# Performance work log

Measured on AMD Instinct MI355X. Metric: run time of the kernel, lower is better.

The kernel has to match this reference:

```python
import jax, jax.numpy as jnp
import numpy as np

R, K, H_IN, W_IN = 512, 17, 56, 56   # rois, keypoints, heatmap size
ROI_H = ROI_W = 96                   # = ceil(BOX_LEN), fixed by construction
BOX_LEN = 95.5                       # all boxes have this side length
A = -0.75                            # PyTorch bicubic coefficient


def _cubic(x):
    x = jnp.abs(x)
    near = ((A + 2.0) * x - (A + 3.0)) * x * x + 1.0
    far = A * (((x - 5.0) * x + 8.0) * x - 4.0)
    return jnp.where(x <= 1.0, near, jnp.where(x < 2.0, far, 0.0))


def _resize_matrix(out_size, in_size):
    """Dense [out,in] bicubic interpolation matrix (align_corners=False, border-replicate)."""
    scale = in_size / out_size
    src = (jnp.arange(out_size, dtype=jnp.float32) + 0.5) * scale - 0.5
    base = jnp.floor(src).astype(jnp.int32)
    taps = base[:, None] + jnp.arange(-1, 3)                      # [out, 4]
    w = _cubic(src[:, None] - taps.astype(jnp.float32))           # weights from unclamped dist
    taps = jnp.clip(taps, 0, in_size - 1)                         # replicate border
    rows = jnp.broadcast_to(jnp.arange(out_size)[:, None], taps.shape)
    return jnp.zeros((out_size, in_size), jnp.float32).at[rows, taps].add(w)


def setup_inputs() -> dict:
    key = jax.random.key(0)
    k1, k2 = jax.random.split(key)
    masks = jax.random.normal(k1, (R, K, H_IN, W_IN), dtype=jnp.float32)
    offs = jax.random.uniform(k2, (R, 2), jnp.float32, 0.0, 400.0)
    # corner format (c0_start, c1_start, c0_end, c1_end); all lengths == BOX_LEN
    boxes = jnp.concatenate([offs, offs + BOX_LEN], axis=1)
    return {"masks": masks, "boxes": boxes}


def reference(masks, boxes):
    My = _resize_matrix(ROI_H, H_IN)   # [ROI_H, H_IN]
    Mx = _resize_matrix(ROI_W, W_IN)   # [ROI_W, W_IN]
    # separable bicubic resize of every ROI heatmap: [R,K,ROI_H,ROI_W]
    roi = jnp.einsum('hi,rkij,wj->rkhw', My, masks, Mx)
    flat = roi.reshape(R, K, ROI_H * ROI_W)
    pos = jnp.argmax(flat, axis=-1)                                # [R,K]
    y = pos // ROI_W
    x = pos % ROI_W
    scores = jnp.take_along_axis(flat, pos[..., None], axis=-1)[..., 0]  # logit at argmax
    len0 = jnp.maximum(boxes[:, 2] - boxes[:, 0], 1.0)
    len1 = jnp.maximum(boxes[:, 3] - boxes[:, 1], 1.0)
    corr0 = (len0 / ROI_H)[:, None]
    corr1 = (len1 / ROI_W)[:, None]
    p0 = (y.astype(jnp.float32) + 0.5) * corr0 + boxes[:, 0:1]
    p1 = (x.astype(jnp.float32) + 0.5) * corr1 + boxes[:, 1:2]
    predictions = jnp.stack([p0, p1, jnp.ones_like(p0)], axis=1)   # [R, n_dim+1, K]
    return predictions, scores
```

## Files before the change

### kernel.cpp

```cpp
#include <hip/hip_runtime.h>

#define R_    512
#define K_    17
#define HIN   56
#define WIN   56
#define OUTS  96
#define NMAP  (R_ * K_)
#define NT    192
#define RST   98
#define TROWS 60

typedef float v2f __attribute__((ext_vector_type(2)));

constexpr float cubic_c(float xin) {
    float x = xin < 0.0f ? -xin : xin;
    const float A = -0.75f;
    if (x <= 1.0f) return ((A + 2.0f) * x - (A + 3.0f)) * x * x + 1.0f;
    if (x < 2.0f)  return A * (((x - 5.0f) * x + 8.0f) * x - 4.0f);
    return 0.0f;
}

struct XTabT {
    float w[OUTS][4];
    int   s[OUTS];
    constexpr XTabT() : w{}, s{} {
        for (int o = 0; o < OUTS; ++o) {
            float src = ((float)o + 0.5f) * (56.0f / 96.0f) - 0.5f;
            int base = (int)src;
            if ((float)base > src) --base;
            int st = base - 1;
            if (st < 0) st = 0;
            if (st > HIN - 4) st = HIN - 4;
            s[o] = st;
            for (int q = 0; q < 4; ++q) {
                int tap = base - 1 + q;
                float wt = cubic_c(src - (float)tap);
                int p = tap < 0 ? 0 : (tap > HIN - 1 ? HIN - 1 : tap);
                w[o][p - st] += wt;
            }
        }
    }
};
constexpr XTabT XT;

struct YTabT {
    float w[12][4];
    int   d[12];
    constexpr YTabT() : w{}, d{} {
        for (int ph = 0; ph < 12; ++ph) {
            float src = ((float)ph + 0.5f) * (56.0f / 96.0f) - 0.5f;
            int base = (int)src;
            if ((float)base > src) --base;
            d[ph] = base - 1;
            for (int q = 0; q < 4; ++q)
                w[ph][q] = cubic_c(src - (float)(base - 1 + q));
        }
    }
};
constexpr YTabT YT;

template<int G>
__device__ __forceinline__ void p1_cols(const float* __restrict__ r0,
                                        const float* __restrict__ r1,
                                        v2f* __restrict__ dst) {
    constexpr int FS = (G == 0) ? 0 : (G == 1) ? 4 : 9;
    constexpr int NF = (G == 1) ? 6 : 5;
    v2f rr[NF * 4];
    const float4* A = (const float4*)r0 + FS;
    const float4* B = (const float4*)r1 + FS;
#pragma unroll
    for (int i = 0; i < NF; ++i) {
        float4 a = A[i], b = B[i];
        rr[4 * i + 0] = (v2f){a.x, b.x};
        rr[4 * i + 1] = (v2f){a.y, b.y};
        rr[4 * i + 2] = (v2f){a.z, b.z};
        rr[4 * i + 3] = (v2f){a.w, b.w};
    }
#pragma unroll
    for (int i = 0; i < 16; ++i) {
        const int o0 = 32 * G + 2 * i, o1 = o0 + 1;
        const int s0 = XT.s[o0] - 4 * FS, s1 = XT.s[o1] - 4 * FS;
        v2f a0 = rr[s0] * (v2f){XT.w[o0][0], XT.w[o0][0]};
        a0 = __builtin_elementwise_fma((v2f){XT.w[o0][1], XT.w[o0][1]}, rr[s0 + 1], a0);
        a0 = __builtin_elementwise_fma((v2f){XT.w[o0][2], XT.w[o0][2]}, rr[s0 + 2], a0);
        a0 = __builtin_elementwise_fma((v2f){XT.w[o0][3], XT.w[o0][3]}, rr[s0 + 3], a0);
        v2f a1 = rr[s1] * (v2f){XT.w[o1][0], XT.w[o1][0]};
        a1 = __builtin_elementwise_fma((v2f){XT.w[o1][1], XT.w[o1][1]}, rr[s1 + 1], a1);
        a1 = __builtin_elementwise_fma((v2f){XT.w[o1][2], XT.w[o1][2]}, rr[s1 + 2], a1);
        a1 = __builtin_elementwise_fma((v2f){XT.w[o1][3], XT.w[o1][3]}, rr[s1 + 3], a1);
        float4 st = {a0.x, a0.y, a1.x, a1.y};
        *(float4*)(dst + 2 * i) = st;
    }
}

__device__ __forceinline__ v2f yv(const v2f* __restrict__ c, int hh) {
    const int ph = hh % 12, b = hh / 12;
    const int i0 = 7 * b + YT.d[ph] + 2;
    v2f acc = c[i0] * (v2f){YT.w[ph][0], YT.w[ph][0]};
    acc = __builtin_elementwise_fma((v2f){YT.w[ph][1], YT.w[ph][1]}, c[i0 + 1], acc);
    acc = __builtin_elementwise_fma((v2f){YT.w[ph][2], YT.w[ph][2]}, c[i0 + 2], acc);
    acc = __builtin_elementwise_fma((v2f){YT.w[ph][3], YT.w[ph][3]}, c[i0 + 3], acc);
    return acc;
}

__global__ __launch_bounds__(NT)
void _Keypointer_kernel(const float* __restrict__ masks,
                        const float* __restrict__ boxes,
                        float* __restrict__ out) {
    __shared__ __align__(16) v2f tmp[TROWS * RST];
    __shared__ v2f wmax[3];
    __shared__ int candp[2];

    const int t   = threadIdx.x;
    const int bm0 = 2 * blockIdx.x;
    const int g   = t >> 6;
    const int w   = t & 63;

    const int srcrow = min(max(w - 2, 0), HIN - 1);
    const int phys   = min(w, TROWS - 1);
    const float* r0 = masks + (size_t)bm0 * (HIN * WIN) + srcrow * WIN;
    const float* r1 = r0 + HIN * WIN;
    v2f* dst = tmp + phys * RST + 32 * g;
    if      (g == 0) p1_cols<0>(r0, r1, dst);
    else if (g == 1) p1_cols<1>(r0, r1, dst);
    else             p1_cols<2>(r0, r1, dst);

    if (t == 0) { candp[0] = 0x7fffffff; candp[1] = 0x7fffffff; }
    __syncthreads();

    const int half = (t >= 96) ? 1 : 0;
    const int col  = t - 96 * half;
    const int h0   = 48 * half;
    const v2f* cb  = tmp + (28 * half) * RST + col;
    v2f c[32];
#pragma unroll
    for (int i = 0; i < 32; ++i) c[i] = cb[i * RST];

    v2f vmax = {-INFINITY, -INFINITY};
#pragma unroll
    for (int hh = 0; hh < 48; ++hh)
        vmax = __builtin_elementwise_max(vmax, yv(c, hh));

    float m0 = vmax.x, m1 = vmax.y;
#pragma unroll
    for (int off = 32; off > 0; off >>= 1) {
        m0 = fmaxf(m0, __shfl_down(m0, off, 64));
        m1 = fmaxf(m1, __shfl_down(m1, off, 64));
    }
    if (w == 0) wmax[g] = (v2f){m0, m1};
    __syncthreads();

    const float M0 = fmaxf(fmaxf(wmax[0].x, wmax[1].x), wmax[2].x);
    const float M1 = fmaxf(fmaxf(wmax[0].y, wmax[1].y), wmax[2].y);

    if (vmax.x == M0 || vmax.y == M1) {
        int c0 = 0x7fffffff, c1 = 0x7fffffff;
#pragma unroll
        for (int hh = 0; hh < 48; ++hh) {
            v2f a = yv(c, hh);
            int fp = (h0 + hh) * OUTS + col;
            if (a.x == M0) c0 = min(c0, fp);
            if (a.y == M1) c1 = min(c1, fp);
        }
        if (c0 != 0x7fffffff) atomicMin(&candp[0], c0);
        if (c1 != 0x7fffffff) atomicMin(&candp[1], c1);
    }
    __syncthreads();

    if (t < 2) {
        const int map = bm0 + t;
        const float M = t ? M1 : M0;
        const int bp  = candp[t];
        const int r = map / K_, k = map - r * K_;
        const int y = bp / OUTS, x = bp - y * OUTS;
        const float b0f = boxes[r * 4 + 0], b1f = boxes[r * 4 + 1];
        const float b2f = boxes[r * 4 + 2], b3f = boxes[r * 4 + 3];
        const float corr0 = fmaxf(b2f - b0f, 1.0f) / (float)OUTS;
        const float corr1 = fmaxf(b3f - b1f, 1.0f) / (float)OUTS;
        const float p0 = ((float)y + 0.5f) * corr0 + b0f;
        const float p1 = ((float)x + 0.5f) * corr1 + b1f;
        out[(r * 3 + 0) * K_ + k] = p0;
        out[(r * 3 + 1) * K_ + k] = p1;
        out[(r * 3 + 2) * K_ + k] = 1.0f;
        out[R_ * 3 * K_ + r * K_ + k] = M;
    }
}

extern "C" void kernel_launch(void* const* d_in, const int* in_sizes, int n_in,
                              void* d_out, int out_size, void* d_ws, size_t ws_size,
                              hipStream_t stream) {
    const float* masks = (const float*)d_in[0];
    const float* boxes = (const float*)d_in[1];
    float* out = (float*)d_out;
    _Keypointer_kernel<<<NMAP / 2, NT, 0, stream>>>(masks, boxes, out);
}
```

Measured before the change: 158.3 us.

## Stage masks through LDS with coalesced loads and process rows in two halves

The kernel now loads both input maps into shared memory with coalesced float4 reads instead of having each thread fetch whole rows straight from global memory. The horizontal pass is split into two 32-row halves that reuse a smaller tmp buffer, and the vertical pass runs in matching halves. Launch bounds ask for 3 blocks per CU. This trades extra syncs and a larger LDS footprint (about 26KB staging plus 25KB tmp) for better global coalescing and fewer registers per thread.

```diff
diff --git a/kernel.cpp b/kernel.cpp
--- a/kernel.cpp
+++ b/kernel.cpp
@@ -8,7 +8,8 @@
 #define NMAP  (R_ * K_)
 #define NT    192
 #define RST   98
-#define TROWS 60
+#define SROW  58
+#define SMAP  (HIN * SROW)
 
 typedef float v2f __attribute__((ext_vector_type(2)));
 
@@ -60,21 +61,23 @@
 constexpr YTabT YT;
 
 template<int G>
-__device__ __forceinline__ void p1_cols(const float* __restrict__ r0,
-                                        const float* __restrict__ r1,
+__device__ __forceinline__ void p1_cols(const float* __restrict__ sa,
+                                        const float* __restrict__ sb,
                                         v2f* __restrict__ dst) {
     constexpr int FS = (G == 0) ? 0 : (G == 1) ? 4 : 9;
     constexpr int NF = (G == 1) ? 6 : 5;
     v2f rr[NF * 4];
-    const float4* A = (const float4*)r0 + FS;
-    const float4* B = (const float4*)r1 + FS;
-#pragma unroll
-    for (int i = 0; i < NF; ++i) {
-        float4 a = A[i], b = B[i];
-        rr[4 * i + 0] = (v2f){a.x, b.x};
-        rr[4 * i + 1] = (v2f){a.y, b.y};
-        rr[4 * i + 2] = (v2f){a.z, b.z};
-        rr[4 * i + 3] = (v2f){a.w, b.w};
+    {
+        float a_[NF * 4], b_[NF * 4];
+#pragma unroll
+        for (int p = 0; p < NF * 2; ++p) {
+            float2 va = *(const float2*)(sa + 2 * p);
+            float2 vb = *(const float2*)(sb + 2 * p);
+            a_[2 * p] = va.x; a_[2 * p + 1] = va.y;
+            b_[2 * p] = vb.x; b_[2 * p + 1] = vb.y;
+        }
+#pragma unroll
+        for (int f = 0; f < NF * 4; ++f) rr[f] = (v2f){a_[f], b_[f]};
     }
 #pragma unroll
     for (int i = 0; i < 16; ++i) {
@@ -88,9 +91,22 @@
         a1 = __builtin_elementwise_fma((v2f){XT.w[o1][1], XT.w[o1][1]}, rr[s1 + 1], a1);
         a1 = __builtin_elementwise_fma((v2f){XT.w[o1][2], XT.w[o1][2]}, rr[s1 + 2], a1);
         a1 = __builtin_elementwise_fma((v2f){XT.w[o1][3], XT.w[o1][3]}, rr[s1 + 3], a1);
-        float4 st = {a0.x, a0.y, a1.x, a1.y};
-        *(float4*)(dst + 2 * i) = st;
-    }
+        *(float4*)(dst + 2 * i) = (float4){a0.x, a0.y, a1.x, a1.y};
+    }
+}
+
+__device__ __forceinline__ void p1_half(const float* __restrict__ stg,
+                                        v2f* __restrict__ tmp, int t, bool low) {
+    const int g = t >> 6;
+    const int w = t & 63;
+    if (w >= 32) return;
+    const int srcrow = low ? max(w - 2, 0) : min(26 + w, HIN - 1);
+    const float* sa = stg + srcrow * SROW + ((g == 0) ? 0 : (g == 1) ? 16 : 36);
+    const float* sb = sa + SMAP;
+    v2f* dst = tmp + w * RST + 32 * g;
+    if      (g == 0) p1_cols<0>(sa, sb, dst);
+    else if (g == 1) p1_cols<1>(sa, sb, dst);
+    else             p1_cols<2>(sa, sb, dst);
 }
 
 __device__ __forceinline__ v2f yv(const v2f* __restrict__ c, int hh) {
@@ -103,43 +119,62 @@
     return acc;
 }
 
-__global__ __launch_bounds__(NT)
+__global__ __launch_bounds__(NT, 3)
 void _Keypointer_kernel(const float* __restrict__ masks,
                         const float* __restrict__ boxes,
                         float* __restrict__ out) {
-    __shared__ __align__(16) v2f tmp[TROWS * RST];
+    __shared__ __align__(16) float stg[2 * SMAP];
+    __shared__ __align__(16) v2f  tmp[32 * RST];
     __shared__ v2f wmax[3];
     __shared__ int candp[2];
 
     const int t   = threadIdx.x;
     const int bm0 = 2 * blockIdx.x;
-    const int g   = t >> 6;
-    const int w   = t & 63;
-
-    const int srcrow = min(max(w - 2, 0), HIN - 1);
-    const int phys   = min(w, TROWS - 1);
-    const float* r0 = masks + (size_t)bm0 * (HIN * WIN) + srcrow * WIN;
-    const float* r1 = r0 + HIN * WIN;
-    v2f* dst = tmp + phys * RST + 32 * g;
-    if      (g == 0) p1_cols<0>(r0, r1, dst);
-    else if (g == 1) p1_cols<1>(r0, r1, dst);
-    else             p1_cols<2>(r0, r1, dst);
-
+
+    {
+        const float4* g4 = (const float4*)(masks + (size_t)bm0 * (HIN * WIN));
+        int u = t, mm = 0, r = t / 14, kk = t % 14;
+#pragma unroll
+        for (int i = 0; i < 9; ++i) {
+            if (i < 8 || u < 1568) {
+                float4 v = g4[u];
+                float* d = stg + mm * SMAP + r * SROW + 4 * kk;
+                *(float2*)(d)     = make_float2(v.x, v.y);
+                *(float2*)(d + 2) = make_float2(v.z, v.w);
+            }
+            u += NT;
+            kk += 10; if (kk >= 14) { kk -= 14; ++r; }
+            r += 13;  if (r >= HIN) { r -= HIN; mm = 1; }
+        }
+    }
     if (t == 0) { candp[0] = 0x7fffffff; candp[1] = 0x7fffffff; }
     __syncthreads();
 
-    const int half = (t >= 96) ? 1 : 0;
-    const int col  = t - 96 * half;
-    const int h0   = 48 * half;
-    const v2f* cb  = tmp + (28 * half) * RST + col;
-    v2f c[32];
-#pragma unroll
-    for (int i = 0; i < 32; ++i) c[i] = cb[i * RST];
+    const int qq  = t / 96;
+    const int col = t - 96 * qq;
+    const v2f* cb = tmp + 14 * qq * RST + col;
+
+    p1_half(stg, tmp, t, true);
+    __syncthreads();
+    v2f c_lo[18];
+#pragma unroll
+    for (int i = 0; i < 18; ++i) c_lo[i] = cb[i * RST];
+    __syncthreads();
+
+    p1_half(stg, tmp, t, false);
 
     v2f vmax = {-INFINITY, -INFINITY};
 #pragma unroll
-    for (int hh = 0; hh < 48; ++hh)
-        vmax = __builtin_elementwise_max(vmax, yv(c, hh));
+    for (int hh = 0; hh < 24; ++hh)
+        vmax = __builtin_elementwise_max(vmax, yv(c_lo, hh));
+    __syncthreads();
+
+    v2f c_hi[18];
+#pragma unroll
+    for (int i = 0; i < 18; ++i) c_hi[i] = cb[i * RST];
+#pragma unroll
+    for (int hh = 0; hh < 24; ++hh)
+        vmax = __builtin_elementwise_max(vmax, yv(c_hi, hh));
 
     float m0 = vmax.x, m1 = vmax.y;
 #pragma unroll
@@ -147,7 +182,7 @@
         m0 = fmaxf(m0, __shfl_down(m0, off, 64));
         m1 = fmaxf(m1, __shfl_down(m1, off, 64));
     }
-    if (w == 0) wmax[g] = (v2f){m0, m1};
+    if ((t & 63) == 0) wmax[t >> 6] = (v2f){m0, m1};
     __syncthreads();
 
     const float M0 = fmaxf(fmaxf(wmax[0].x, wmax[1].x), wmax[2].x);
@@ -156,9 +191,16 @@
     if (vmax.x == M0 || vmax.y == M1) {
         int c0 = 0x7fffffff, c1 = 0x7fffffff;
 #pragma unroll
-        for (int hh = 0; hh < 48; ++hh) {
-            v2f a = yv(c, hh);
-            int fp = (h0 + hh) * OUTS + col;
+        for (int hh = 0; hh < 24; ++hh) {
+            v2f a = yv(c_lo, hh);
+            int fp = (24 * qq + hh) * OUTS + col;
+            if (a.x == M0) c0 = min(c0, fp);
+            if (a.y == M1) c1 = min(c1, fp);
+        }
+#pragma unroll
+        for (int hh = 0; hh < 24; ++hh) {
+            v2f a = yv(c_hi, hh);
+            int fp = (48 + 24 * qq + hh) * OUTS + col;
             if (a.x == M0) c0 = min(c0, fp);
             if (a.y == M1) c1 = min(c1, fp);
         }
```

Result: slower. 169.0 us (+6.7%).

## Process four map pairs per block with register prefetch of next pair

Applied to the files above, without the earlier changes.

Each block now loops over four map pairs, loading the next pair's mask rows into registers while computing the current pair's horizontal pass and argmax. Barriers are replaced by a lighter LDS-only waitcnt+barrier, and launch bounds request two blocks per CU. This aims to hide global load latency and amortise block launch overhead, at the cost of a quarter as many blocks and more register pressure.

```diff
diff --git a/kernel.cpp b/kernel.cpp
--- a/kernel.cpp
+++ b/kernel.cpp
@@ -8,9 +8,18 @@
 #define NMAP  (R_ * K_)
 #define NT    192
 #define RST   98
-#define TROWS 60
+#define MAPSZ (HIN * WIN)
+#define PAIRS 4
+#define NBLK  (NMAP / (2 * PAIRS))
 
 typedef float v2f __attribute__((ext_vector_type(2)));
+
+__device__ __forceinline__ void bar_lds() {
+    asm volatile("" ::: "memory");
+    __builtin_amdgcn_s_waitcnt(0xc07f);
+    __builtin_amdgcn_s_barrier();
+    asm volatile("" ::: "memory");
+}
 
 constexpr float cubic_c(float xin) {
     float x = xin < 0.0f ? -xin : xin;
@@ -60,26 +69,11 @@
 constexpr YTabT YT;
 
 template<int G>
-__device__ __forceinline__ void p1_cols(const float* __restrict__ r0,
-                                        const float* __restrict__ r1,
-                                        v2f* __restrict__ dst) {
-    constexpr int FS = (G == 0) ? 0 : (G == 1) ? 4 : 9;
-    constexpr int NF = (G == 1) ? 6 : 5;
-    v2f rr[NF * 4];
-    const float4* A = (const float4*)r0 + FS;
-    const float4* B = (const float4*)r1 + FS;
-#pragma unroll
-    for (int i = 0; i < NF; ++i) {
-        float4 a = A[i], b = B[i];
-        rr[4 * i + 0] = (v2f){a.x, b.x};
-        rr[4 * i + 1] = (v2f){a.y, b.y};
-        rr[4 * i + 2] = (v2f){a.z, b.z};
-        rr[4 * i + 3] = (v2f){a.w, b.w};
-    }
+__device__ __forceinline__ void p1fma(const v2f (&rr)[24], v2f* __restrict__ dst) {
 #pragma unroll
     for (int i = 0; i < 16; ++i) {
         const int o0 = 32 * G + 2 * i, o1 = o0 + 1;
-        const int s0 = XT.s[o0] - 4 * FS, s1 = XT.s[o1] - 4 * FS;
+        const int s0 = XT.s[o0] - 16 * G, s1 = XT.s[o1] - 16 * G;
         v2f a0 = rr[s0] * (v2f){XT.w[o0][0], XT.w[o0][0]};
         a0 = __builtin_elementwise_fma((v2f){XT.w[o0][1], XT.w[o0][1]}, rr[s0 + 1], a0);
         a0 = __builtin_elementwise_fma((v2f){XT.w[o0][2], XT.w[o0][2]}, rr[s0 + 2], a0);
@@ -88,8 +82,7 @@
         a1 = __builtin_elementwise_fma((v2f){XT.w[o1][1], XT.w[o1][1]}, rr[s1 + 1], a1);
         a1 = __builtin_elementwise_fma((v2f){XT.w[o1][2], XT.w[o1][2]}, rr[s1 + 2], a1);
         a1 = __builtin_elementwise_fma((v2f){XT.w[o1][3], XT.w[o1][3]}, rr[s1 + 3], a1);
-        float4 st = {a0.x, a0.y, a1.x, a1.y};
-        *(float4*)(dst + 2 * i) = st;
+        *(float4*)(dst + 2 * i) = (float4){a0.x, a0.y, a1.x, a1.y};
     }
 }
 
@@ -103,86 +96,104 @@
     return acc;
 }
 
-__global__ __launch_bounds__(NT)
+__global__ __launch_bounds__(NT, 2)
 void _Keypointer_kernel(const float* __restrict__ masks,
                         const float* __restrict__ boxes,
                         float* __restrict__ out) {
-    __shared__ __align__(16) v2f tmp[TROWS * RST];
+    __shared__ __align__(16) v2f tmp[60 * RST];
     __shared__ v2f wmax[3];
     __shared__ int candp[2];
 
-    const int t   = threadIdx.x;
-    const int bm0 = 2 * blockIdx.x;
-    const int g   = t >> 6;
-    const int w   = t & 63;
-
+    const int t = threadIdx.x;
+    const int g = t >> 6;
+    const int w = t & 63;
     const int srcrow = min(max(w - 2, 0), HIN - 1);
-    const int phys   = min(w, TROWS - 1);
-    const float* r0 = masks + (size_t)bm0 * (HIN * WIN) + srcrow * WIN;
-    const float* r1 = r0 + HIN * WIN;
-    v2f* dst = tmp + phys * RST + 32 * g;
-    if      (g == 0) p1_cols<0>(r0, r1, dst);
-    else if (g == 1) p1_cols<1>(r0, r1, dst);
-    else             p1_cols<2>(r0, r1, dst);
-
-    if (t == 0) { candp[0] = 0x7fffffff; candp[1] = 0x7fffffff; }
-    __syncthreads();
-
-    const int half = (t >= 96) ? 1 : 0;
-    const int col  = t - 96 * half;
-    const int h0   = 48 * half;
-    const v2f* cb  = tmp + (28 * half) * RST + col;
-    v2f c[32];
-#pragma unroll
-    for (int i = 0; i < 32; ++i) c[i] = cb[i * RST];
-
-    v2f vmax = {-INFINITY, -INFINITY};
-#pragma unroll
-    for (int hh = 0; hh < 48; ++hh)
-        vmax = __builtin_elementwise_max(vmax, yv(c, hh));
-
-    float m0 = vmax.x, m1 = vmax.y;
-#pragma unroll
-    for (int off = 32; off > 0; off >>= 1) {
-        m0 = fmaxf(m0, __shfl_down(m0, off, 64));
-        m1 = fmaxf(m1, __shfl_down(m1, off, 64));
-    }
-    if (w == 0) wmax[g] = (v2f){m0, m1};
-    __syncthreads();
-
-    const float M0 = fmaxf(fmaxf(wmax[0].x, wmax[1].x), wmax[2].x);
-    const float M1 = fmaxf(fmaxf(wmax[0].y, wmax[1].y), wmax[2].y);
-
-    if (vmax.x == M0 || vmax.y == M1) {
-        int c0 = 0x7fffffff, c1 = 0x7fffffff;
-#pragma unroll
-        for (int hh = 0; hh < 48; ++hh) {
-            v2f a = yv(c, hh);
-            int fp = (h0 + hh) * OUTS + col;
-            if (a.x == M0) c0 = min(c0, fp);
-            if (a.y == M1) c1 = min(c1, fp);
-        }
-        if (c0 != 0x7fffffff) atomicMin(&candp[0], c0);
-        if (c1 != 0x7fffffff) atomicMin(&candp[1], c1);
-    }
-    __syncthreads();
-
-    if (t < 2) {
-        const int map = bm0 + t;
-        const float M = t ? M1 : M0;
-        const int bp  = candp[t];
-        const int r = map / K_, k = map - r * K_;
-        const int y = bp / OUTS, x = bp - y * OUTS;
-        const float b0f = boxes[r * 4 + 0], b1f = boxes[r * 4 + 1];
-        const float b2f = boxes[r * 4 + 2], b3f = boxes[r * 4 + 3];
-        const float corr0 = fmaxf(b2f - b0f, 1.0f) / (float)OUTS;
-        const float corr1 = fmaxf(b3f - b1f, 1.0f) / (float)OUTS;
-        const float p0 = ((float)y + 0.5f) * corr0 + b0f;
-        const float p1 = ((float)x + 0.5f) * corr1 + b1f;
-        out[(r * 3 + 0) * K_ + k] = p0;
-        out[(r * 3 + 1) * K_ + k] = p1;
-        out[(r * 3 + 2) * K_ + k] = 1.0f;
-        out[R_ * 3 * K_ + r * K_ + k] = M;
+    const int phys   = min(w, 59);
+    const int half   = (t >= 96) ? 1 : 0;
+    const int col    = t - 96 * half;
+    const v2f* cb    = tmp + 28 * half * RST + col;
+    v2f* dst         = tmp + phys * RST + 32 * g;
+
+    const int pair0 = PAIRS * blockIdx.x;
+    const float4* gp = (const float4*)(masks + (size_t)(2 * pair0) * MAPSZ
+                                       + srcrow * WIN) + 4 * g;
+
+    if (t < 2) candp[t] = 0x7fffffff;
+
+    float4 pa[6], pb[6];
+#pragma unroll
+    for (int i = 0; i < 6; ++i) { pa[i] = gp[i]; pb[i] = gp[MAPSZ / 4 + i]; }
+
+#pragma unroll 1
+    for (int it = 0; it < PAIRS; ++it) {
+        v2f rr[24];
+#pragma unroll
+        for (int i = 0; i < 6; ++i) {
+            rr[4 * i + 0] = (v2f){pa[i].x, pb[i].x};
+            rr[4 * i + 1] = (v2f){pa[i].y, pb[i].y};
+            rr[4 * i + 2] = (v2f){pa[i].z, pb[i].z};
+            rr[4 * i + 3] = (v2f){pa[i].w, pb[i].w};
+        }
+        if (it + 1 < PAIRS) {
+            gp += 2 * (MAPSZ / 4);
+#pragma unroll
+            for (int i = 0; i < 6; ++i) { pa[i] = gp[i]; pb[i] = gp[MAPSZ / 4 + i]; }
+        }
+        if      (g == 0) p1fma<0>(rr, dst);
+        else if (g == 1) p1fma<1>(rr, dst);
+        else             p1fma<2>(rr, dst);
+        bar_lds();
+
+        v2f c[32];
+#pragma unroll
+        for (int i = 0; i < 32; ++i) c[i] = cb[i * RST];
+        v2f vm = {-INFINITY, -INFINITY};
+#pragma unroll
+        for (int hh = 0; hh < 48; ++hh)
+            vm = __builtin_elementwise_max(vm, yv(c, hh));
+
+        float m0 = vm.x, m1 = vm.y;
+#pragma unroll
+        for (int off = 32; off > 0; off >>= 1) {
+            m0 = fmaxf(m0, __shfl_down(m0, off, 64));
+            m1 = fmaxf(m1, __shfl_down(m1, off, 64));
+        }
+        if (w == 0) wmax[g] = (v2f){m0, m1};
+        bar_lds();
+
+        const float M0 = fmaxf(fmaxf(wmax[0].x, wmax[1].x), wmax[2].x);
+        const float M1 = fmaxf(fmaxf(wmax[0].y, wmax[1].y), wmax[2].y);
+
+        if (vm.x == M0 || vm.y == M1) {
+            int c0 = 0x7fffffff, c1 = 0x7fffffff;
+#pragma unroll
+            for (int hh = 0; hh < 48; ++hh) {
+                v2f a = yv(c, hh);
+                int fp = (48 * half + hh) * OUTS + col;
+                if (a.x == M0) c0 = min(c0, fp);
+                if (a.y == M1) c1 = min(c1, fp);
+            }
+            if (c0 != 0x7fffffff) atomicMin(&candp[0], c0);
+            if (c1 != 0x7fffffff) atomicMin(&candp[1], c1);
+        }
+        bar_lds();
+
+        if (t < 2) {
+            const int map = 2 * (pair0 + it) + t;
+            const float M = t ? M1 : M0;
+            const int bp = candp[t];
+            candp[t] = 0x7fffffff;
+            const int r = map / K_, k = map - r * K_;
+            const int y = bp / OUTS, x = bp - y * OUTS;
+            const float b0f = boxes[r * 4 + 0], b1f = boxes[r * 4 + 1];
+            const float b2f = boxes[r * 4 + 2], b3f = boxes[r * 4 + 3];
+            const float corr0 = fmaxf(b2f - b0f, 1.0f) / (float)OUTS;
+            const float corr1 = fmaxf(b3f - b1f, 1.0f) / (float)OUTS;
+            out[(r * 3 + 0) * K_ + k] = ((float)y + 0.5f) * corr0 + b0f;
+            out[(r * 3 + 1) * K_ + k] = ((float)x + 0.5f) * corr1 + b1f;
+            out[(r * 3 + 2) * K_ + k] = 1.0f;
+            out[R_ * 3 * K_ + r * K_ + k] = M;
+        }
     }
 }
 
@@ -192,5 +203,5 @@
     const float* masks = (const float*)d_in[0];
     const float* boxes = (const float*)d_in[1];
     float* out = (float*)d_out;
-    _Keypointer_kernel<<<NMAP / 2, NT, 0, stream>>>(masks, boxes, out);
-}
+    _Keypointer_kernel<<<NBLK, NT, 0, stream>>>(masks, boxes, out);
+}
```

After: 178.5 us. 1.13x slower.
